# Kernel optimization log

Hardware: AMD Instinct MI355X
Metric: run time of the kernel (lower is better)

The kernel has to match this reference:

```python
import jax, jax.numpy as jnp
import numpy as np

# Model dims (match init_kwargs)
D_MODEL = 1024
D_INNER = 2048
D_STATE = 16
D_CONV = 4
DT_RANK = 64
H = 8                      # num_heads
P = D_INNER // H           # head_dim = 256
DT_MIN, DT_MAX = 1e-4, 1.0
BATCH, SEQ = 2, 4096
TOTAL_OUT = 2 * D_INNER + DT_RANK + 2 * H * D_STATE  # 4416 (no gated delta)
EPS = 1e-6


def _xavier(k, shape):
    fan_out, fan_in = shape
    return jax.random.normal(k, shape, jnp.float32) * np.sqrt(2.0 / (fan_in + fan_out))


def setup_inputs() -> dict:
    key = jax.random.key(0)
    ks = jax.random.split(key, 8)
    x = jax.random.normal(ks[0], (BATCH, SEQ, D_MODEL), jnp.float32)
    W_in = _xavier(ks[1], (TOTAL_OUT, D_MODEL))          # in_proj (no bias)
    W_dt = _xavier(ks[2], (H, DT_RANK))                  # dt_proj (no bias)
    conv_w = jax.random.normal(ks[3], (D_INNER, D_CONV), jnp.float32) * 0.1
    conv_b = jnp.zeros((D_INNER,), jnp.float32)
    # A_log init: log(1..d_state) per head
    A_log = jnp.broadcast_to(jnp.log(jnp.arange(1, D_STATE + 1, dtype=jnp.float32)), (H, D_STATE))
    Dskip = jnp.ones((H, P), jnp.float32)
    # dt_bias = inverse_softplus(dt), dt log-uniform in [dt_min, dt_max]
    dt0 = jnp.exp(jax.random.uniform(ks[4], (H,), jnp.float32)
                  * (np.log(DT_MAX) - np.log(DT_MIN)) + np.log(DT_MIN))
    dt_bias = dt0 + jnp.log(-jnp.expm1(-dt0))
    norm_w = jnp.ones((D_INNER,), jnp.float32)
    W_out = _xavier(ks[5], (D_MODEL, D_INNER))
    W_res = _xavier(ks[6], (D_INNER, D_MODEL))           # residual_proj (d_model != d_inner)
    return dict(x=x, W_in=W_in, W_dt=W_dt, conv_w=conv_w, conv_b=conv_b,
                A_log=A_log, Dskip=Dskip, dt_bias=dt_bias, norm_w=norm_w,
                W_out=W_out, W_res=W_res)


def _causal_dwconv(u, w, b):
    # u: (B,L,C) -> causal depthwise conv along L. w: (C,K), b: (C,)
    lhs = u.transpose(0, 2, 1)               # (B,C,L)
    rhs = w[:, None, :]                      # (C,1,K)
    out = jax.lax.conv_general_dilated(
        lhs, rhs, window_strides=(1,), padding=[(D_CONV - 1, 0)],
        dimension_numbers=('NCH', 'OIH', 'NCH'), feature_group_count=D_INNER)
    return (out + b[None, :, None]).transpose(0, 2, 1)


def reference(x, W_in, W_dt, conv_w, conv_b, A_log, Dskip, dt_bias, norm_w, W_out, W_res):
    Bsz, L, _ = x.shape
    p = x @ W_in.T                                            # (B,L,TOTAL_OUT)
    splits = np.cumsum([D_INNER, D_INNER, DT_RANK, H * D_STATE]).tolist()
    z, u, dt_h, Bf, Cf = jnp.split(p, splits, axis=-1)
    Bp = Bf.reshape(Bsz, L, H, D_STATE)
    Cp = Cf.reshape(Bsz, L, H, D_STATE)
    u = _causal_dwconv(u, conv_w, conv_b)                     # (B,L,D_INNER)
    # dt_prep: softplus(dt_raw + bias) clamped to [dt_min, dt_max]
    dt = jnp.clip(jax.nn.softplus(dt_h @ W_dt.T + dt_bias), DT_MIN, DT_MAX)  # (B,L,H)
    A = -jnp.exp(A_log)                                       # (H,N)
    uh = u.reshape(Bsz, L, H, P)

    def step(h, inp):
        u_t, dt_t, B_t, C_t = inp                             # (B,H,P),(B,H),(B,H,N),(B,H,N)
        dA = jnp.exp(dt_t[..., None] * A)                     # (B,H,N)
        h = h * dA[:, :, None, :] + (dt_t[:, :, None, None] * u_t[..., None]) * B_t[:, :, None, :]
        y_t = jnp.einsum('bhpn,bhn->bhp', h, C_t)
        return h, y_t

    h0 = jnp.zeros((Bsz, H, P, D_STATE), x.dtype)
    xs = (uh.transpose(1, 0, 2, 3), dt.transpose(1, 0, 2),
          Bp.transpose(1, 0, 2, 3), Cp.transpose(1, 0, 2, 3))
    _, ys = jax.lax.scan(step, h0, xs)                        # (L,B,H,P)
    y = ys.transpose(1, 0, 2, 3) + Dskip[None, None] * uh     # skip connection
    y = y.reshape(Bsz, L, D_INNER)

    residual_inner = x @ W_res.T                              # residual_proj
    # fused_out: g = RMSNorm(y * silu(z) + residual) * weight
    g = y * jax.nn.silu(z) + residual_inner
    g = g * jax.lax.rsqrt(jnp.mean(g * g, axis=-1, keepdims=True) + EPS) * norm_w
    return g @ W_out.T
```

## Files before the change

### kernel.cpp

```cpp
#include <hip/hip_runtime.h>
#include <hip/hip_bf16.h>
#include <math.h>

#define DMODEL  1024
#define DINNER  2048
#define DSTATE  16
#define DCONV   4
#define DTRANK  64
#define NH      8
#define PH      256
#define TOTOUT  4416
#define NTOT2   6528
#define MB_ROWS 4096
#define LC      64
#define NCB     (MB_ROWS/LC)

typedef __attribute__((ext_vector_type(8))) short bf16x8;
typedef __attribute__((ext_vector_type(4))) float f32x4;

__device__ inline unsigned cvt2bf(float lo, float hi) {
    unsigned r;
    asm("v_cvt_pk_bf16_f32 %0, %1, %2" : "=v"(r) : "v"(lo), "v"(hi));
    return r;
}
__device__ inline ushort f2bf(float v) { return (ushort)(cvt2bf(v, v) & 0xffffu); }
__device__ inline float bf2f(ushort u) {
    union { unsigned u; float f; } w; w.u = (unsigned)u << 16; return w.f;
}
__device__ inline void gload16(const ushort* g, ushort* l) {
    __builtin_amdgcn_global_load_lds((const __attribute__((address_space(1))) unsigned*)(const void*)g,
                                     (__attribute__((address_space(3))) unsigned*)(void*)l, 16, 0, 0);
}

__global__ __launch_bounds__(256) void cvt_all(const float* __restrict__ W_in,
                                               const float* __restrict__ W_res,
                                               const float* __restrict__ W_out,
                                               const float* __restrict__ norm_w,
                                               const float* __restrict__ x,
                                               ushort* __restrict__ WB,
                                               ushort* __restrict__ XBF) {
    const size_t E_WCAT = (size_t)NTOT2 * DMODEL;
    const size_t E_WOUT = E_WCAT + (size_t)DMODEL * DINNER;
    size_t i = ((size_t)blockIdx.x * 256 + threadIdx.x) * 8;
    const float* src;
    ushort* dst;
    bool zero = false, scale = false;
    size_t k0 = 0;
    if (i < E_WCAT) {
        size_t r = i >> 10, c = i & 1023;
        if (r < 4096)       src = W_in + (r << 10) + c;
        else if (r < 6144)  src = W_res + ((r - 4096) << 10) + c;
        else if (r < 6464)  src = W_in + ((r - 2048) << 10) + c;
        else { src = W_in; zero = true; }
        dst = WB + i;
    } else if (i < E_WOUT) {
        size_t o = i - E_WCAT;
        src = W_out + o;
        dst = WB + i;
        scale = true;
        k0 = o & (DINNER - 1);
    } else {
        src = x + (i - E_WOUT);
        dst = XBF + (i - E_WOUT);
    }
    float4 v0, v1;
    if (zero) { v0 = make_float4(0.f, 0.f, 0.f, 0.f); v1 = v0; }
    else { v0 = *(const float4*)src; v1 = *(const float4*)(src + 4); }
    if (scale) {
        float4 n0 = *(const float4*)(norm_w + k0);
        float4 n1 = *(const float4*)(norm_w + k0 + 4);
        v0.x *= n0.x; v0.y *= n0.y; v0.z *= n0.z; v0.w *= n0.w;
        v1.x *= n1.x; v1.y *= n1.y; v1.z *= n1.z; v1.w *= n1.w;
    }
    uint4 o;
    o.x = cvt2bf(v0.x, v0.y); o.y = cvt2bf(v0.z, v0.w);
    o.z = cvt2bf(v1.x, v1.y); o.w = cvt2bf(v1.z, v1.w);
    *(uint4*)dst = o;
}

__global__ __launch_bounds__(512) void gemm_fused(const ushort* __restrict__ A,
                                                  const ushort* __restrict__ W,
                                                  ushort* __restrict__ Zb,
                                                  ushort* __restrict__ Ub,
                                                  ushort* __restrict__ RESb,
                                                  float* __restrict__ DBCp,
                                                  int ntx, int K) {
    __shared__ __align__(16) ushort L[3 * 12288];
    const int nwg  = gridDim.x;
    const int orig = blockIdx.x;
    const int swz  = (orig & 7) * (nwg >> 3) + (orig >> 3);
    const int bx = swz % ntx, by = swz / ntx;
    const int row0 = by * 256, col0 = bx * 128;

    const int t    = threadIdx.x;
    const int lane = t & 63, w = t >> 6;
    const int wr   = w >> 1, wc = w & 1;
    const int l15  = lane & 15, l4 = lane >> 4;

    const int r0g = t >> 2, s0g = t & 3;
    const int r1g = r0g + 128;
    const int rr0 = r0g ^ ((r0g >> 3) & 1), cc0 = s0g ^ ((r0g >> 1) & 3);
    const int rr1 = r1g ^ ((r1g >> 3) & 1), cc1 = s0g ^ ((r1g >> 1) & 3);
    const ushort* sA0 = A + (size_t)(row0 + rr0) * K + cc0 * 8;
    const ushort* sA1 = A + (size_t)(row0 + rr1) * K + cc1 * 8;
    const ushort* sB0 = W + (size_t)(col0 + rr0) * K + cc0 * 8;

    int offA[4], offB[4];
    #pragma unroll
    for (int mi = 0; mi < 4; mi++) {
        int rq = wr * 64 + mi * 16 + l15;
        offA[mi] = (rq * 32 + l4 * 8) ^ (((rq >> 1) & 7) << 3);
    }
    #pragma unroll
    for (int ni = 0; ni < 4; ni++) {
        int rq = wc * 64 + ni * 16 + l15;
        offB[ni] = 8192 + ((rq * 32 + l4 * 8) ^ (((rq >> 1) & 7) << 3));
    }

    f32x4 acc[4][4];
    #pragma unroll
    for (int i = 0; i < 4; i++)
        #pragma unroll
        for (int j = 0; j < 4; j++)
            acc[i][j] = (f32x4){0.f, 0.f, 0.f, 0.f};

    const int KT = K >> 5;
    gload16(sA0,      &L[t * 8]);
    gload16(sA1,      &L[4096 + t * 8]);
    gload16(sB0,      &L[8192 + t * 8]);
    gload16(sA0 + 32, &L[12288 + t * 8]);
    gload16(sA1 + 32, &L[12288 + 4096 + t * 8]);
    gload16(sB0 + 32, &L[12288 + 8192 + t * 8]);
    asm volatile("s_waitcnt vmcnt(3)" ::: "memory");
    __builtin_amdgcn_sched_barrier(0);
    __builtin_amdgcn_s_barrier();
    __builtin_amdgcn_sched_barrier(0);

    for (int kt = 0; kt < KT; ++kt) {
        const bool pre = (kt + 2) < KT;
        if (pre) {
            ushort* bp2 = &L[((kt + 2) % 3) * 12288];
            const int ko = (kt + 2) << 5;
            gload16(sA0 + ko, bp2 + t * 8);
            gload16(sA1 + ko, bp2 + 4096 + t * 8);
            gload16(sB0 + ko, bp2 + 8192 + t * 8);
        }
        const ushort* bp = &L[(kt % 3) * 12288];
        bf16x8 af[4], bw[4];
        #pragma unroll
        for (int mi = 0; mi < 4; mi++) af[mi] = *(const bf16x8*)(bp + offA[mi]);
        #pragma unroll
        for (int ni = 0; ni < 4; ni++) bw[ni] = *(const bf16x8*)(bp + offB[ni]);
        __builtin_amdgcn_s_setprio(1);
        #pragma unroll
        for (int mi = 0; mi < 4; mi++)
            #pragma unroll
            for (int ni = 0; ni < 4; ni++)
                acc[mi][ni] = __builtin_amdgcn_mfma_f32_16x16x32_bf16(af[mi], bw[ni], acc[mi][ni], 0, 0, 0);
        __builtin_amdgcn_s_setprio(0);
        if (pre) { asm volatile("s_waitcnt vmcnt(3)" ::: "memory"); }
        else     { asm volatile("s_waitcnt vmcnt(0)" ::: "memory"); }
        __builtin_amdgcn_sched_barrier(0);
        __builtin_amdgcn_s_barrier();
        __builtin_amdgcn_sched_barrier(0);
    }

    #pragma unroll
    for (int mi = 0; mi < 4; mi++) {
        #pragma unroll
        for (int ni = 0; ni < 4; ni++) {
            #pragma unroll
            for (int rr = 0; rr < 4; rr++) {
                const int row = row0 + wr * 64 + mi * 16 + l4 * 4 + rr;
                const int col = col0 + wc * 64 + ni * 16 + l15;
                const float v = acc[mi][ni][rr];
                if (col0 < DINNER) {
                    Zb[(size_t)row * DINNER + col] = f2bf(v);
                } else if (col0 < 2 * DINNER) {
                    Ub[(size_t)row * DINNER + (col - DINNER)] = f2bf(v);
                } else if (col0 < 3 * DINNER) {
                    RESb[(size_t)row * DINNER + (col - 2 * DINNER)] = f2bf(v);
                } else {
                    if (col < 3 * DINNER + 320)
                        DBCp[(size_t)row * 320 + (col - 3 * DINNER)] = v;
                }
            }
        }
    }
}

__global__ __launch_bounds__(256) void gemm_out128(const ushort* __restrict__ A,
                                                   const ushort* __restrict__ W,
                                                   const float* __restrict__ ssqp,
                                                   float* __restrict__ C0,
                                                   int ntx, int K, int ldc) {
    __shared__ __align__(16) ushort L[3 * 8192];
    const int nwg  = gridDim.x;
    const int orig = blockIdx.x;
    const int swz  = (orig & 7) * (nwg >> 3) + (orig >> 3);
    const int bx = swz % ntx, by = swz / ntx;
    const int row0 = by * 128, col0 = bx * 128;

    const int t    = threadIdx.x;
    const int lane = t & 63, w = t >> 6;
    const int wr   = w >> 1, wc = w & 1;
    const int l15  = lane & 15, l4 = lane >> 4;

    const int r0g = t >> 2, s0g = t & 3;
    const int r1g = r0g + 64;
    const int rr0 = r0g ^ ((r0g >> 3) & 1), cc0 = s0g ^ ((r0g >> 1) & 3);
    const int rr1 = r1g ^ ((r1g >> 3) & 1), cc1 = s0g ^ ((r1g >> 1) & 3);
    const ushort* sA0 = A + (size_t)(row0 + rr0) * K + cc0 * 8;
    const ushort* sA1 = A + (size_t)(row0 + rr1) * K + cc1 * 8;
    const ushort* sB0 = W + (size_t)(col0 + rr0) * K + cc0 * 8;
    const ushort* sB1 = W + (size_t)(col0 + rr1) * K + cc1 * 8;

    int offA[4], offB[4];
    #pragma unroll
    for (int mi = 0; mi < 4; mi++) {
        int rq = wr * 64 + mi * 16 + l15;
        offA[mi] = (rq * 32 + l4 * 8) ^ (((rq >> 1) & 7) << 3);
    }
    #pragma unroll
    for (int ni = 0; ni < 4; ni++) {
        int rq = wc * 64 + ni * 16 + l15;
        offB[ni] = 4096 + ((rq * 32 + l4 * 8) ^ (((rq >> 1) & 7) << 3));
    }

    f32x4 acc[4][4];
    #pragma unroll
    for (int i = 0; i < 4; i++)
        #pragma unroll
        for (int j = 0; j < 4; j++)
            acc[i][j] = (f32x4){0.f, 0.f, 0.f, 0.f};

    const int KT = K >> 5;
    gload16(sA0,      &L[t * 8]);
    gload16(sA1,      &L[2048 + t * 8]);
    gload16(sB0,      &L[4096 + t * 8]);
    gload16(sB1,      &L[6144 + t * 8]);
    gload16(sA0 + 32, &L[8192 + t * 8]);
    gload16(sA1 + 32, &L[8192 + 2048 + t * 8]);
    gload16(sB0 + 32, &L[8192 + 4096 + t * 8]);
    gload16(sB1 + 32, &L[8192 + 6144 + t * 8]);
    asm volatile("s_waitcnt vmcnt(4)" ::: "memory");
    __builtin_amdgcn_sched_barrier(0);
    __builtin_amdgcn_s_barrier();
    __builtin_amdgcn_sched_barrier(0);

    for (int kt = 0; kt < KT; ++kt) {
        const bool pre = (kt + 2) < KT;
        if (pre) {
            ushort* bp2 = &L[((kt + 2) % 3) * 8192];
            const int ko = (kt + 2) << 5;
            gload16(sA0 + ko, bp2 + t * 8);
            gload16(sA1 + ko, bp2 + 2048 + t * 8);
            gload16(sB0 + ko, bp2 + 4096 + t * 8);
            gload16(sB1 + ko, bp2 + 6144 + t * 8);
        }
        const ushort* bp = &L[(kt % 3) * 8192];
        bf16x8 af[4], bw[4];
        #pragma unroll
        for (int mi = 0; mi < 4; mi++) af[mi] = *(const bf16x8*)(bp + offA[mi]);
        #pragma unroll
        for (int ni = 0; ni < 4; ni++) bw[ni] = *(const bf16x8*)(bp + offB[ni]);
        __builtin_amdgcn_s_setprio(1);
        #pragma unroll
        for (int mi = 0; mi < 4; mi++)
            #pragma unroll
            for (int ni = 0; ni < 4; ni++)
                acc[mi][ni] = __builtin_amdgcn_mfma_f32_16x16x32_bf16(af[mi], bw[ni], acc[mi][ni], 0, 0, 0);
        __builtin_amdgcn_s_setprio(0);
        if (pre) { asm volatile("s_waitcnt vmcnt(4)" ::: "memory"); }
        else     { asm volatile("s_waitcnt vmcnt(0)" ::: "memory"); }
        __builtin_amdgcn_sched_barrier(0);
        __builtin_amdgcn_s_barrier();
        __builtin_amdgcn_sched_barrier(0);
    }

    float inv[4][4];
    #pragma unroll
    for (int mi = 0; mi < 4; mi++)
        #pragma unroll
        for (int rr = 0; rr < 4; rr++) {
            const int row = row0 + wr * 64 + mi * 16 + l4 * 4 + rr;
            const float* p = ssqp + (size_t)row * 8;
            float s = ((p[0] + p[1]) + (p[2] + p[3])) + ((p[4] + p[5]) + (p[6] + p[7]));
            inv[mi][rr] = rsqrtf(s * (1.f / (float)DINNER) + 1e-6f);
        }

    #pragma unroll
    for (int mi = 0; mi < 4; mi++)
        #pragma unroll
        for (int ni = 0; ni < 4; ni++)
            #pragma unroll
            for (int rr = 0; rr < 4; rr++) {
                const int row = row0 + wr * 64 + mi * 16 + l4 * 4 + rr;
                const int col = col0 + wc * 64 + ni * 16 + l15;
                C0[(size_t)row * ldc + col] = acc[mi][ni][rr] * inv[mi][rr];
            }
}

__global__ __launch_bounds__(256) void scan_local(const ushort* __restrict__ Ub,
                                                  const float* __restrict__ DBC,
                                                  const float* __restrict__ W_dt,
                                                  const float* __restrict__ dt_bias,
                                                  const float* __restrict__ A_log,
                                                  const float* __restrict__ cw,
                                                  const float* __restrict__ cb,
                                                  float* __restrict__ hloc,
                                                  float* __restrict__ Pc) {
    const int c = blockIdx.x, h = blockIdx.y;
    const int pidx = threadIdx.x;
    const int ch = h * PH + pidx;
    const int t0 = c * LC;
    __shared__ float sdt[LC];
    __shared__ float sdA[LC][DSTATE];
    __shared__ float sdB[LC][DSTATE];
    const int st = pidx >> 4, sn = pidx & 15;

    if (pidx < LC) {
        const float* row = DBC + (size_t)(t0 + pidx) * 320;
        const float* wd = W_dt + h * DTRANK;
        float acc = dt_bias[h];
        #pragma unroll 16
        for (int r2 = 0; r2 < DTRANK; r2++) acc = fmaf(row[r2], wd[r2], acc);
        float sp = acc > 20.f ? acc : log1pf(expf(acc));
        sdt[pidx] = fminf(fmaxf(sp, 1e-4f), 1.0f);
    }
    const float w0 = cw[ch * 4], w1 = cw[ch * 4 + 1], w2 = cw[ch * 4 + 2], w3 = cw[ch * 4 + 3];
    const float bia = cb[ch];
    const int bs = (c / NCB) * MB_ROWS;
    float um3 = (t0 - 3 >= bs) ? bf2f(Ub[(size_t)(t0 - 3) * DINNER + ch]) : 0.f;
    float um2 = (t0 - 2 >= bs) ? bf2f(Ub[(size_t)(t0 - 2) * DINNER + ch]) : 0.f;
    float um1 = (t0 - 1 >= bs) ? bf2f(Ub[(size_t)(t0 - 1) * DINNER + ch]) : 0.f;
    __syncthreads();

    {
        const float nA = -expf(A_log[h * DSTATE + sn]);
        #pragma unroll
        for (int j = 0; j < 4; j++) {
            int tt = st + j * 16;
            size_t trow = (size_t)(t0 + tt);
            float dv = sdt[tt];
            sdA[tt][sn] = expf(dv * nA);
            sdB[tt][sn] = dv * DBC[trow * 320 + 64 + h * DSTATE + sn];
        }
    }
    __syncthreads();

    float hst[DSTATE] = {};
    for (int t = 0; t < LC; t++) {
        float u0 = bf2f(Ub[(size_t)(t0 + t) * DINNER + ch]);
        float up = fmaf(w3, u0, fmaf(w2, um1, fmaf(w1, um2, fmaf(w0, um3, bia))));
        um3 = um2; um2 = um1; um1 = u0;
        #pragma unroll
        for (int n = 0; n < DSTATE; n++)
            hst[n] = fmaf(hst[n], sdA[t][n], up * sdB[t][n]);
    }
    float* hl = hloc + (((size_t)c * NH + h) * PH + pidx) * DSTATE;
    #pragma unroll
    for (int n = 0; n < DSTATE; n++) hl[n] = hst[n];

    if (pidx < DSTATE) {
        float pr = 1.f;
        for (int t = 0; t < LC; t++) pr *= sdA[t][pidx];
        Pc[((size_t)c * NH + h) * DSTATE + pidx] = pr;
    }
}

__global__ __launch_bounds__(256) void scan_carry(const float* __restrict__ hloc,
                                                  const float* __restrict__ Pc,
                                                  float* __restrict__ Hent) {
    int g = blockIdx.x * 256 + threadIdx.x;
    int b = g >> 15;
    int r = g & 32767;
    int h = r >> 12;
    int inner = r & 4095;
    int n = r & 15;
    float carry = 0.f;
    for (int i = 0; i < NCB; i++) {
        int c = b * NCB + i;
        size_t idx = ((size_t)c * NH + h) * (PH * DSTATE) + inner;
        Hent[idx] = carry;
        carry = fmaf(Pc[((size_t)c * NH + h) * DSTATE + n], carry, hloc[idx]);
    }
}

__global__ __launch_bounds__(256) void scan_out(const ushort* __restrict__ Zb,
                                                const ushort* __restrict__ Ub,
                                                const ushort* __restrict__ RESb,
                                                ushort* __restrict__ Yb,
                                                float* __restrict__ ssqp,
                                                const float* __restrict__ DBC,
                                                const float* __restrict__ W_dt,
                                                const float* __restrict__ dt_bias,
                                                const float* __restrict__ A_log,
                                                const float* __restrict__ cw,
                                                const float* __restrict__ cb,
                                                const float* __restrict__ Dskip,
                                                const float* __restrict__ Hent) {
    const int c = blockIdx.x, h = blockIdx.y;
    const int pidx = threadIdx.x;
    const int ch = h * PH + pidx;
    const int t0 = c * LC;
    const int wv = pidx >> 6, lane = pidx & 63;
    __shared__ float sdt[LC];
    __shared__ float sdA[LC][DSTATE];
    __shared__ float sdB[LC][DSTATE];
    __shared__ float sC [LC][DSTATE];
    __shared__ float sred[LC][4];
    const int st = pidx >> 4, sn = pidx & 15;

    if (pidx < LC) {
        const float* row = DBC + (size_t)(t0 + pidx) * 320;
        const float* wd = W_dt + h * DTRANK;
        float acc = dt_bias[h];
        #pragma unroll 16
        for (int r2 = 0; r2 < DTRANK; r2++) acc = fmaf(row[r2], wd[r2], acc);
        float sp = acc > 20.f ? acc : log1pf(expf(acc));
        sdt[pidx] = fminf(fmaxf(sp, 1e-4f), 1.0f);
    }
    const float w0 = cw[ch * 4], w1 = cw[ch * 4 + 1], w2 = cw[ch * 4 + 2], w3 = cw[ch * 4 + 3];
    const float bia = cb[ch];
    const int bs = (c / NCB) * MB_ROWS;
    float um3 = (t0 - 3 >= bs) ? bf2f(Ub[(size_t)(t0 - 3) * DINNER + ch]) : 0.f;
    float um2 = (t0 - 2 >= bs) ? bf2f(Ub[(size_t)(t0 - 2) * DINNER + ch]) : 0.f;
    float um1 = (t0 - 1 >= bs) ? bf2f(Ub[(size_t)(t0 - 1) * DINNER + ch]) : 0.f;
    __syncthreads();

    {
        const float nA = -expf(A_log[h * DSTATE + sn]);
        #pragma unroll
        for (int j = 0; j < 4; j++) {
            int tt = st + j * 16;
            size_t trow = (size_t)(t0 + tt);
            float dv = sdt[tt];
            sdA[tt][sn] = expf(dv * nA);
            sdB[tt][sn] = dv * DBC[trow * 320 + 64 + h * DSTATE + sn];
            sC [tt][sn] =      DBC[trow * 320 + 192 + h * DSTATE + sn];
        }
    }
    const float dsk = Dskip[ch];
    float hst[DSTATE];
    const float* he = Hent + (((size_t)c * NH + h) * PH + pidx) * DSTATE;
    #pragma unroll
    for (int n = 0; n < DSTATE; n++) hst[n] = he[n];
    __syncthreads();

    for (int t = 0; t < LC; t++) {
        size_t off = (size_t)(t0 + t) * DINNER + ch;
        float u0 = bf2f(Ub[off]);
        float up = fmaf(w3, u0, fmaf(w2, um1, fmaf(w1, um2, fmaf(w0, um3, bia))));
        um3 = um2; um2 = um1; um1 = u0;
        float a0 = 0.f, a1 = 0.f, a2 = 0.f, a3 = 0.f;
        #pragma unroll
        for (int n = 0; n < 4; n++) {
            hst[n +  0] = fmaf(hst[n +  0], sdA[t][n +  0], up * sdB[t][n +  0]);
            hst[n +  4] = fmaf(hst[n +  4], sdA[t][n +  4], up * sdB[t][n +  4]);
            hst[n +  8] = fmaf(hst[n +  8], sdA[t][n +  8], up * sdB[t][n +  8]);
            hst[n + 12] = fmaf(hst[n + 12], sdA[t][n + 12], up * sdB[t][n + 12]);
            a0 = fmaf(hst[n +  0], sC[t][n +  0], a0);
            a1 = fmaf(hst[n +  4], sC[t][n +  4], a1);
            a2 = fmaf(hst[n +  8], sC[t][n +  8], a2);
            a3 = fmaf(hst[n + 12], sC[t][n + 12], a3);
        }
        float yv = ((a0 + a1) + (a2 + a3)) + dsk * up;
        float zv = bf2f(Zb[off]);
        float sil = zv / (1.f + expf(-zv));
        float gv = fmaf(yv, sil, bf2f(RESb[off]));
        Yb[off] = f2bf(gv);
        float ss = gv * gv;
        #pragma unroll
        for (int o2 = 32; o2 > 0; o2 >>= 1) ss += __shfl_down(ss, o2);
        if (lane == 0) sred[t][wv] = ss;
    }
    __syncthreads();
    if (pidx < LC) {
        float s4 = (sred[pidx][0] + sred[pidx][1]) + (sred[pidx][2] + sred[pidx][3]);
        ssqp[(size_t)(t0 + pidx) * 8 + h] = s4;
    }
}

struct Lay {
    float *DBC, *PC, *HLOC, *HENT, *SSQP;
    ushort *YB, *ZB, *UB, *RESB, *XBF, *WB;
    size_t total;
};
static Lay mk_layout(char* base, int Mr) {
    size_t o = 0;
    auto take = [&](size_t bytes) { char* p = base + o; o = (o + bytes + 255) & ~(size_t)255; return p; };
    Lay l;
    l.YB   = (ushort*)take((size_t)Mr * 2048 * 2);
    l.DBC  = (float*) take((size_t)Mr * 320 * 4);
    l.PC   = (float*) take((size_t)(Mr / 64) * NH * DSTATE * 4);
    l.HLOC = (float*) take((size_t)Mr * 512 * 4);
    l.HENT = (float*) take((size_t)Mr * 512 * 4);
    l.SSQP = (float*) take((size_t)Mr * 8 * 4);
    l.ZB   = (ushort*)take((size_t)Mr * 2048 * 2);
    l.UB   = (ushort*)take((size_t)Mr * 2048 * 2);
    l.RESB = (ushort*)take((size_t)Mr * 2048 * 2);
    l.XBF  = (ushort*)take((size_t)8192 * 1024 * 2);
    l.WB   = (ushort*)take(((size_t)NTOT2 * 1024 + (size_t)1024 * 2048) * 2);
    l.total = o;
    return l;
}

extern "C" void kernel_launch(void* const* d_in, const int* in_sizes, int n_in,
                              void* d_out, int out_size, void* d_ws, size_t ws_size,
                              hipStream_t stream) {
    const float* x       = (const float*)d_in[0];
    const float* W_in    = (const float*)d_in[1];
    const float* W_dt    = (const float*)d_in[2];
    const float* conv_w  = (const float*)d_in[3];
    const float* conv_b  = (const float*)d_in[4];
    const float* A_log   = (const float*)d_in[5];
    const float* Dskip   = (const float*)d_in[6];
    const float* dt_bias = (const float*)d_in[7];
    const float* norm_w  = (const float*)d_in[8];
    const float* W_out   = (const float*)d_in[9];
    const float* W_res   = (const float*)d_in[10];
    float* out = (float*)d_out;

    Lay probe = mk_layout(nullptr, 2 * MB_ROWS);
    const bool fat = ws_size >= probe.total;
    const int Mr = fat ? 2 * MB_ROWS : MB_ROWS;
    const int npass = fat ? 1 : 2;
    const int nbc = fat ? 2 : 1;
    Lay l = mk_layout((char*)d_ws, Mr);

    ushort* wcat = l.WB;
    ushort* wotb = wcat + (size_t)NTOT2 * 1024;

    {
        const size_t total_gran = ((size_t)NTOT2 * 1024 + (size_t)1024 * 2048 + (size_t)8192 * 1024) / 8;
        cvt_all<<<(int)(total_gran / 256), 256, 0, stream>>>(W_in, W_res, W_out, norm_w, x, l.WB, l.XBF);
    }

    for (int b = 0; b < npass; b++) {
        const ushort* xb = l.XBF + (size_t)b * MB_ROWS * DMODEL;
        float* outb = out + (size_t)b * MB_ROWS * DMODEL;

        gemm_fused<<<51 * (Mr / 256), 512, 0, stream>>>(xb, wcat, l.ZB, l.UB, l.RESB, l.DBC, 51, DMODEL);
        scan_local<<<dim3(Mr / LC, NH), 256, 0, stream>>>(l.UB, l.DBC, W_dt, dt_bias, A_log,
                                                          conv_w, conv_b, l.HLOC, l.PC);
        scan_carry<<<nbc * 128, 256, 0, stream>>>(l.HLOC, l.PC, l.HENT);
        scan_out<<<dim3(Mr / LC, NH), 256, 0, stream>>>(l.ZB, l.UB, l.RESB, l.YB, l.SSQP, l.DBC,
                                                        W_dt, dt_bias, A_log,
                                                        conv_w, conv_b, Dskip, l.HENT);
        gemm_out128<<<8 * (Mr / 128), 256, 0, stream>>>(l.YB, wotb, l.SSQP, outb, 8, DINNER, DMODEL);
    }
}
```

Baseline: 298.0 us.

## Process two channels per thread and two heads per block in scan kernels

Each thread in scan_local and scan_out now handles two adjacent channels, and each block covers two heads, which halves the grid along the head axis. Each LDS read of dA/dB/C is reused for two state updates, and global loads and stores become vectorized ushort2/float4 accesses. The cost is more registers per thread (two 16-wide state arrays) and fewer blocks, which may lower occupancy and latency hiding.

```diff
diff --git a/kernel.cpp b/kernel.cpp
--- a/kernel.cpp
+++ b/kernel.cpp
@@ -310,62 +310,78 @@
                                                   const float* __restrict__ cb,
                                                   float* __restrict__ hloc,
                                                   float* __restrict__ Pc) {
-    const int c = blockIdx.x, h = blockIdx.y;
+    const int c = blockIdx.x, hp = blockIdx.y;
     const int pidx = threadIdx.x;
-    const int ch = h * PH + pidx;
+    const int hh = pidx >> 7;
+    const int h  = hp * 2 + hh;
+    const int li = pidx & 127;
+    const int ch = h * PH + li * 2;
     const int t0 = c * LC;
-    __shared__ float sdt[LC];
-    __shared__ float sdA[LC][DSTATE];
-    __shared__ float sdB[LC][DSTATE];
-    const int st = pidx >> 4, sn = pidx & 15;
-
-    if (pidx < LC) {
-        const float* row = DBC + (size_t)(t0 + pidx) * 320;
-        const float* wd = W_dt + h * DTRANK;
-        float acc = dt_bias[h];
+    __shared__ float sdt[2][LC];
+    __shared__ float sdA[2][LC][DSTATE];
+    __shared__ float sdB[2][LC][DSTATE];
+
+    if (pidx < 128) {
+        const int hh2 = pidx >> 6, tt = pidx & 63;
+        const int h2 = hp * 2 + hh2;
+        const float* row = DBC + (size_t)(t0 + tt) * 320;
+        const float* wd = W_dt + h2 * DTRANK;
+        float acc = dt_bias[h2];
         #pragma unroll 16
         for (int r2 = 0; r2 < DTRANK; r2++) acc = fmaf(row[r2], wd[r2], acc);
         float sp = acc > 20.f ? acc : log1pf(expf(acc));
-        sdt[pidx] = fminf(fmaxf(sp, 1e-4f), 1.0f);
-    }
-    const float w0 = cw[ch * 4], w1 = cw[ch * 4 + 1], w2 = cw[ch * 4 + 2], w3 = cw[ch * 4 + 3];
-    const float bia = cb[ch];
+        sdt[hh2][tt] = fminf(fmaxf(sp, 1e-4f), 1.0f);
+    }
+    const float4 cwa = *(const float4*)(cw + ch * 4);
+    const float4 cwb = *(const float4*)(cw + ch * 4 + 4);
+    const float2 cbv = *(const float2*)(cb + ch);
     const int bs = (c / NCB) * MB_ROWS;
-    float um3 = (t0 - 3 >= bs) ? bf2f(Ub[(size_t)(t0 - 3) * DINNER + ch]) : 0.f;
-    float um2 = (t0 - 2 >= bs) ? bf2f(Ub[(size_t)(t0 - 2) * DINNER + ch]) : 0.f;
-    float um1 = (t0 - 1 >= bs) ? bf2f(Ub[(size_t)(t0 - 1) * DINNER + ch]) : 0.f;
+    float um3a = 0.f, um2a = 0.f, um1a = 0.f, um3b = 0.f, um2b = 0.f, um1b = 0.f;
+    if (t0 - 3 >= bs) { ushort2 v = *(const ushort2*)(Ub + (size_t)(t0 - 3) * DINNER + ch); um3a = bf2f(v.x); um3b = bf2f(v.y); }
+    if (t0 - 2 >= bs) { ushort2 v = *(const ushort2*)(Ub + (size_t)(t0 - 2) * DINNER + ch); um2a = bf2f(v.x); um2b = bf2f(v.y); }
+    if (t0 - 1 >= bs) { ushort2 v = *(const ushort2*)(Ub + (size_t)(t0 - 1) * DINNER + ch); um1a = bf2f(v.x); um1b = bf2f(v.y); }
     __syncthreads();
 
     {
+        const int sn = li & 15, stt = li >> 4;
         const float nA = -expf(A_log[h * DSTATE + sn]);
         #pragma unroll
-        for (int j = 0; j < 4; j++) {
-            int tt = st + j * 16;
+        for (int j = 0; j < 8; j++) {
+            int tt = stt + j * 8;
             size_t trow = (size_t)(t0 + tt);
-            float dv = sdt[tt];
-            sdA[tt][sn] = expf(dv * nA);
-            sdB[tt][sn] = dv * DBC[trow * 320 + 64 + h * DSTATE + sn];
+            float dv = sdt[hh][tt];
+            sdA[hh][tt][sn] = expf(dv * nA);
+            sdB[hh][tt][sn] = dv * DBC[trow * 320 + 64 + h * DSTATE + sn];
         }
     }
     __syncthreads();
 
-    float hst[DSTATE] = {};
+    float ha[DSTATE] = {}, hb[DSTATE] = {};
     for (int t = 0; t < LC; t++) {
-        float u0 = bf2f(Ub[(size_t)(t0 + t) * DINNER + ch]);
-        float up = fmaf(w3, u0, fmaf(w2, um1, fmaf(w1, um2, fmaf(w0, um3, bia))));
-        um3 = um2; um2 = um1; um1 = u0;
-        #pragma unroll
-        for (int n = 0; n < DSTATE; n++)
-            hst[n] = fmaf(hst[n], sdA[t][n], up * sdB[t][n]);
-    }
-    float* hl = hloc + (((size_t)c * NH + h) * PH + pidx) * DSTATE;
-    #pragma unroll
-    for (int n = 0; n < DSTATE; n++) hl[n] = hst[n];
-
-    if (pidx < DSTATE) {
+        ushort2 uv = *(const ushort2*)(Ub + (size_t)(t0 + t) * DINNER + ch);
+        float u0a = bf2f(uv.x), u0b = bf2f(uv.y);
+        float upa = fmaf(cwa.w, u0a, fmaf(cwa.z, um1a, fmaf(cwa.y, um2a, fmaf(cwa.x, um3a, cbv.x))));
+        float upb = fmaf(cwb.w, u0b, fmaf(cwb.z, um1b, fmaf(cwb.y, um2b, fmaf(cwb.x, um3b, cbv.y))));
+        um3a = um2a; um2a = um1a; um1a = u0a;
+        um3b = um2b; um2b = um1b; um1b = u0b;
+        #pragma unroll
+        for (int n = 0; n < DSTATE; n++) {
+            float dA = sdA[hh][t][n], dB = sdB[hh][t][n];
+            ha[n] = fmaf(ha[n], dA, upa * dB);
+            hb[n] = fmaf(hb[n], dA, upb * dB);
+        }
+    }
+    float4* hl = (float4*)(hloc + (((size_t)c * NH + h) * PH + li * 2) * DSTATE);
+    #pragma unroll
+    for (int q = 0; q < 4; q++) hl[q]     = make_float4(ha[q*4], ha[q*4+1], ha[q*4+2], ha[q*4+3]);
+    #pragma unroll
+    for (int q = 0; q < 4; q++) hl[4 + q] = make_float4(hb[q*4], hb[q*4+1], hb[q*4+2], hb[q*4+3]);
+
+    if (pidx < 32) {
+        int hh4 = pidx >> 4, n = pidx & 15;
         float pr = 1.f;
-        for (int t = 0; t < LC; t++) pr *= sdA[t][pidx];
-        Pc[((size_t)c * NH + h) * DSTATE + pidx] = pr;
+        for (int t = 0; t < LC; t++) pr *= sdA[hh4][t][n];
+        Pc[((size_t)c * NH + hp * 2 + hh4) * DSTATE + n] = pr;
     }
 }
 
@@ -400,85 +416,108 @@
                                                 const float* __restrict__ cb,
                                                 const float* __restrict__ Dskip,
                                                 const float* __restrict__ Hent) {
-    const int c = blockIdx.x, h = blockIdx.y;
+    const int c = blockIdx.x, hp = blockIdx.y;
     const int pidx = threadIdx.x;
-    const int ch = h * PH + pidx;
+    const int hh = pidx >> 7;
+    const int h  = hp * 2 + hh;
+    const int li = pidx & 127;
+    const int ch = h * PH + li * 2;
     const int t0 = c * LC;
     const int wv = pidx >> 6, lane = pidx & 63;
-    __shared__ float sdt[LC];
-    __shared__ float sdA[LC][DSTATE];
-    __shared__ float sdB[LC][DSTATE];
-    __shared__ float sC [LC][DSTATE];
+    __shared__ float sdt[2][LC];
+    __shared__ float sdA[2][LC][DSTATE];
+    __shared__ float sdB[2][LC][DSTATE];
+    __shared__ float sC [2][LC][DSTATE];
     __shared__ float sred[LC][4];
-    const int st = pidx >> 4, sn = pidx & 15;
-
-    if (pidx < LC) {
-        const float* row = DBC + (size_t)(t0 + pidx) * 320;
-        const float* wd = W_dt + h * DTRANK;
-        float acc = dt_bias[h];
+
+    if (pidx < 128) {
+        const int hh2 = pidx >> 6, tt = pidx & 63;
+        const int h2 = hp * 2 + hh2;
+        const float* row = DBC + (size_t)(t0 + tt) * 320;
+        const float* wd = W_dt + h2 * DTRANK;
+        float acc = dt_bias[h2];
         #pragma unroll 16
         for (int r2 = 0; r2 < DTRANK; r2++) acc = fmaf(row[r2], wd[r2], acc);
         float sp = acc > 20.f ? acc : log1pf(expf(acc));
-        sdt[pidx] = fminf(fmaxf(sp, 1e-4f), 1.0f);
-    }
-    const float w0 = cw[ch * 4], w1 = cw[ch * 4 + 1], w2 = cw[ch * 4 + 2], w3 = cw[ch * 4 + 3];
-    const float bia = cb[ch];
+        sdt[hh2][tt] = fminf(fmaxf(sp, 1e-4f), 1.0f);
+    }
+    const float4 cwa = *(const float4*)(cw + ch * 4);
+    const float4 cwb = *(const float4*)(cw + ch * 4 + 4);
+    const float2 cbv = *(const float2*)(cb + ch);
+    const float2 dskv = *(const float2*)(Dskip + ch);
     const int bs = (c / NCB) * MB_ROWS;
-    float um3 = (t0 - 3 >= bs) ? bf2f(Ub[(size_t)(t0 - 3) * DINNER + ch]) : 0.f;
-    float um2 = (t0 - 2 >= bs) ? bf2f(Ub[(size_t)(t0 - 2) * DINNER + ch]) : 0.f;
-    float um1 = (t0 - 1 >= bs) ? bf2f(Ub[(size_t)(t0 - 1) * DINNER + ch]) : 0.f;
+    float um3a = 0.f, um2a = 0.f, um1a = 0.f, um3b = 0.f, um2b = 0.f, um1b = 0.f;
+    if (t0 - 3 >= bs) { ushort2 v = *(const ushort2*)(Ub + (size_t)(t0 - 3) * DINNER + ch); um3a = bf2f(v.x); um3b = bf2f(v.y); }
+    if (t0 - 2 >= bs) { ushort2 v = *(const ushort2*)(Ub + (size_t)(t0 - 2) * DINNER + ch); um2a = bf2f(v.x); um2b = bf2f(v.y); }
+    if (t0 - 1 >= bs) { ushort2 v = *(const ushort2*)(Ub + (size_t)(t0 - 1) * DINNER + ch); um1a = bf2f(v.x); um1b = bf2f(v.y); }
     __syncthreads();
 
     {
+        const int sn = li & 15, stt = li >> 4;
         const float nA = -expf(A_log[h * DSTATE + sn]);
         #pragma unroll
-        for (int j = 0; j < 4; j++) {
-            int tt = st + j * 16;
+        for (int j = 0; j < 8; j++) {
+            int tt = stt + j * 8;
             size_t trow = (size_t)(t0 + tt);
-            float dv = sdt[tt];
-            sdA[tt][sn] = expf(dv * nA);
-            sdB[tt][sn] = dv * DBC[trow * 320 + 64 + h * DSTATE + sn];
-            sC [tt][sn] =      DBC[trow * 320 + 192 + h * DSTATE + sn];
-        }
-    }
-    const float dsk = Dskip[ch];
-    float hst[DSTATE];
-    const float* he = Hent + (((size_t)c * NH + h) * PH + pidx) * DSTATE;
-    #pragma unroll
-    for (int n = 0; n < DSTATE; n++) hst[n] = he[n];
+            float dv = sdt[hh][tt];
+            sdA[hh][tt][sn] = expf(dv * nA);
+            sdB[hh][tt][sn] = dv * DBC[trow * 320 + 64 + h * DSTATE + sn];
+            sC [hh][tt][sn] =      DBC[trow * 320 + 192 + h * DSTATE + sn];
+        }
+    }
+    float ha[DSTATE], hb[DSTATE];
+    {
+        const float4* he = (const float4*)(Hent + (((size_t)c * NH + h) * PH + li * 2) * DSTATE);
+        #pragma unroll
+        for (int q = 0; q < 4; q++) {
+            float4 v = he[q];
+            ha[q*4] = v.x; ha[q*4+1] = v.y; ha[q*4+2] = v.z; ha[q*4+3] = v.w;
+        }
+        #pragma unroll
+        for (int q = 0; q < 4; q++) {
+            float4 v = he[4 + q];
+            hb[q*4] = v.x; hb[q*4+1] = v.y; hb[q*4+2] = v.z; hb[q*4+3] = v.w;
+        }
+    }
     __syncthreads();
 
     for (int t = 0; t < LC; t++) {
         size_t off = (size_t)(t0 + t) * DINNER + ch;
-        float u0 = bf2f(Ub[off]);
-        float up = fmaf(w3, u0, fmaf(w2, um1, fmaf(w1, um2, fmaf(w0, um3, bia))));
-        um3 = um2; um2 = um1; um1 = u0;
-        float a0 = 0.f, a1 = 0.f, a2 = 0.f, a3 = 0.f;
-        #pragma unroll
-        for (int n = 0; n < 4; n++) {
-            hst[n +  0] = fmaf(hst[n +  0], sdA[t][n +  0], up * sdB[t][n +  0]);
-            hst[n +  4] = fmaf(hst[n +  4], sdA[t][n +  4], up * sdB[t][n +  4]);
-            hst[n +  8] = fmaf(hst[n +  8], sdA[t][n +  8], up * sdB[t][n +  8]);
-            hst[n + 12] = fmaf(hst[n + 12], sdA[t][n + 12], up * sdB[t][n + 12]);
-            a0 = fmaf(hst[n +  0], sC[t][n +  0], a0);
-            a1 = fmaf(hst[n +  4], sC[t][n +  4], a1);
-            a2 = fmaf(hst[n +  8], sC[t][n +  8], a2);
-            a3 = fmaf(hst[n + 12], sC[t][n + 12], a3);
-        }
-        float yv = ((a0 + a1) + (a2 + a3)) + dsk * up;
-        float zv = bf2f(Zb[off]);
-        float sil = zv / (1.f + expf(-zv));
-        float gv = fmaf(yv, sil, bf2f(RESb[off]));
-        Yb[off] = f2bf(gv);
-        float ss = gv * gv;
+        ushort2 uv = *(const ushort2*)(Ub + off);
+        float u0a = bf2f(uv.x), u0b = bf2f(uv.y);
+        float upa = fmaf(cwa.w, u0a, fmaf(cwa.z, um1a, fmaf(cwa.y, um2a, fmaf(cwa.x, um3a, cbv.x))));
+        float upb = fmaf(cwb.w, u0b, fmaf(cwb.z, um1b, fmaf(cwb.y, um2b, fmaf(cwb.x, um3b, cbv.y))));
+        um3a = um2a; um2a = um1a; um1a = u0a;
+        um3b = um2b; um2b = um1b; um1b = u0b;
+        float aa = 0.f, ab = 0.f;
+        #pragma unroll
+        for (int n = 0; n < DSTATE; n++) {
+            float dA = sdA[hh][t][n], dB = sdB[hh][t][n], dC = sC[hh][t][n];
+            ha[n] = fmaf(ha[n], dA, upa * dB);
+            hb[n] = fmaf(hb[n], dA, upb * dB);
+            aa = fmaf(ha[n], dC, aa);
+            ab = fmaf(hb[n], dC, ab);
+        }
+        float ya = fmaf(dskv.x, upa, aa);
+        float yb = fmaf(dskv.y, upb, ab);
+        ushort2 zv2 = *(const ushort2*)(Zb + off);
+        ushort2 rv2 = *(const ushort2*)(RESb + off);
+        float za = bf2f(zv2.x), zb2 = bf2f(zv2.y);
+        float sa = za / (1.f + expf(-za));
+        float sb = zb2 / (1.f + expf(-zb2));
+        float ga = fmaf(ya, sa, bf2f(rv2.x));
+        float gb = fmaf(yb, sb, bf2f(rv2.y));
+        *(unsigned*)(Yb + off) = cvt2bf(ga, gb);
+        float ss = fmaf(gb, gb, ga * ga);
         #pragma unroll
         for (int o2 = 32; o2 > 0; o2 >>= 1) ss += __shfl_down(ss, o2);
         if (lane == 0) sred[t][wv] = ss;
     }
     __syncthreads();
-    if (pidx < LC) {
-        float s4 = (sred[pidx][0] + sred[pidx][1]) + (sred[pidx][2] + sred[pidx][3]);
-        ssqp[(size_t)(t0 + pidx) * 8 + h] = s4;
+    if (pidx < 128) {
+        int hh5 = pidx >> 6, rr = pidx & 63;
+        float s = sred[rr][hh5 * 2] + sred[rr][hh5 * 2 + 1];
+        ssqp[(size_t)(t0 + rr) * 8 + hp * 2 + hh5] = s;
     }
 }
 
@@ -542,12 +581,12 @@
         float* outb = out + (size_t)b * MB_ROWS * DMODEL;
 
         gemm_fused<<<51 * (Mr / 256), 512, 0, stream>>>(xb, wcat, l.ZB, l.UB, l.RESB, l.DBC, 51, DMODEL);
-        scan_local<<<dim3(Mr / LC, NH), 256, 0, stream>>>(l.UB, l.DBC, W_dt, dt_bias, A_log,
-                                                          conv_w, conv_b, l.HLOC, l.PC);
+        scan_local<<<dim3(Mr / LC, NH / 2), 256, 0, stream>>>(l.UB, l.DBC, W_dt, dt_bias, A_log,
+                                                              conv_w, conv_b, l.HLOC, l.PC);
         scan_carry<<<nbc * 128, 256, 0, stream>>>(l.HLOC, l.PC, l.HENT);
-        scan_out<<<dim3(Mr / LC, NH), 256, 0, stream>>>(l.ZB, l.UB, l.RESB, l.YB, l.SSQP, l.DBC,
-                                                        W_dt, dt_bias, A_log,
-                                                        conv_w, conv_b, Dskip, l.HENT);
+        scan_out<<<dim3(Mr / LC, NH / 2), 256, 0, stream>>>(l.ZB, l.UB, l.RESB, l.YB, l.SSQP, l.DBC,
+                                                            W_dt, dt_bias, A_log,
+                                                            conv_w, conv_b, Dskip, l.HENT);
         gemm_out128<<<8 * (Mr / 128), 256, 0, stream>>>(l.YB, wotb, l.SSQP, outb, 8, DINNER, DMODEL);
     }
 }
```

New measurement: 299.8 us. Within noise of the previous version (+0.6%).
